# Kernel tuning notes

Measured on AMD Instinct MI355X. Metric: run time of the kernel, lower is better.

The kernel has to match this reference:

```python
import jax, jax.numpy as jnp
import numpy as np

N = 4096        # batch size (rows)
K = 4           # instances per class -> num_instances in the torch code
D = 256         # embedding dim
MARGIN = 0.5
SAMPLE_KEY = jax.random.key(42)  # fixed key: deterministic stand-in for torch.multinomial


def setup_inputs() -> dict:
    key = jax.random.key(0)
    x = jax.random.normal(key, (N, D), dtype=jnp.float32)
    # L2-normalize like typical metric-learning embeddings so sims are in [-1, 1]
    inputs = x / jnp.linalg.norm(x, axis=1, keepdims=True)
    targets = (jnp.arange(N) // K).astype(jnp.int32)  # P*K batch: equal-size classes
    return {"inputs": inputs, "targets": targets}


def reference(inputs, targets):
    n = inputs.shape[0]
    km1 = K - 1                 # positives per row
    n_neg = n - K               # negatives per row

    sim = inputs @ inputs.T                                   # [n, n]
    same = targets[:, None] == targets[None, :]
    eye = jnp.eye(n, dtype=bool)
    pos_mask = same & ~eye
    neg_mask = ~same

    # masked_select + per-row sort: masked entries -> +inf, ascending sort,
    # keep first count entries (counts are uniform across rows)
    pos_sorted = jnp.sort(jnp.where(pos_mask, sim, jnp.inf), axis=1)[:, :km1]   # [n, K-1]
    neg_sorted = jnp.sort(jnp.where(neg_mask, sim, jnp.inf), axis=1)[:, :n_neg] # [n, n-K]

    pos_d = jnp.mean(pos_sorted)
    neg_d = jnp.mean(neg_sorted)

    # GaussDistribution per row over negatives
    neg_mean = jnp.mean(neg_sorted, axis=1, keepdims=True)
    neg_std = jnp.sqrt(jnp.mean((neg_sorted - neg_mean) ** 2, axis=1, keepdims=True))
    # NOTE: the original uses exp(+(x-mu)^2 / (2 sigma^2)) (no minus sign) -- faithful
    logprob = (neg_sorted - neg_mean) ** 2 / (2.0 * neg_std ** 2)               # [n, n-K]

    # multinomial without replacement ~ Gumbel top-k on log-weights
    gumbel = -jnp.log(-jnp.log(
        jax.random.uniform(SAMPLE_KEY, logprob.shape, minval=1e-20, maxval=1.0)))
    _, neg_idx = jax.lax.top_k(logprob + gumbel, km1)                            # [n, K-1]
    neg_pair = jnp.take_along_axis(neg_sorted, neg_idx, axis=1)                  # [n, K-1]

    pos_loss = jnp.mean(jnp.log1p(jnp.exp(-2.0 * (pos_sorted - MARGIN))), axis=1)
    neg_loss = 0.04 * jnp.mean(jnp.log1p(jnp.exp(50.0 * (neg_pair - MARGIN))), axis=1)
    loss = jnp.sum(pos_loss + neg_loss) / n

    # prec: fraction of rows where hardest positive > hardest sampled negative + 0.05
    c = jnp.sum(pos_sorted[:, -1] > jnp.max(neg_pair, axis=1) + 0.05)
    prec = c.astype(jnp.float32) / n

    return loss, prec, pos_d, neg_d
```

## Files before the change

kernel.cpp:

```cpp
#include <hip/hip_runtime.h>
#include <hip/hip_bf16.h>
#include <cstdint>
#include <cfloat>
#include <math.h>

#define NN 4096
#define DD 256
#define NNEG 4092
#define MARGIN 0.5f
#define NB 3584
#define NW (NB / 2)
#define GTOTAL ((uint32_t)NN * (uint32_t)NNEG)

__device__ __forceinline__ uint32_t rotl32(uint32_t x, int r) {
  return (x << r) | (x >> (32 - r));
}

__device__ __forceinline__ void threefry2x32_42(uint32_t x0, uint32_t x1,
                                                uint32_t& o0, uint32_t& o1) {
  const uint32_t k0 = 0u, k1 = 42u;
  const uint32_t k2 = k0 ^ k1 ^ 0x1BD11BDAu;
  x0 += k0; x1 += k1;
#define TF_R(r) { x0 += x1; x1 = rotl32(x1, r); x1 ^= x0; }
  TF_R(13) TF_R(15) TF_R(26) TF_R(6)
  x0 += k1; x1 += k2 + 1u;
  TF_R(17) TF_R(29) TF_R(16) TF_R(24)
  x0 += k2; x1 += k0 + 2u;
  TF_R(13) TF_R(15) TF_R(26) TF_R(6)
  x0 += k0; x1 += k1 + 3u;
  TF_R(17) TF_R(29) TF_R(16) TF_R(24)
  x0 += k1; x1 += k2 + 4u;
  TF_R(13) TF_R(15) TF_R(26) TF_R(6)
  x0 += k2; x1 += k0 + 5u;
#undef TF_R
  o0 = x0; o1 = x1;
}

__device__ __forceinline__ float gumbel_at(uint32_t f) {
  uint32_t o0, o1;
  threefry2x32_42(0u, f, o0, o1);
  uint32_t bits = o0 ^ o1;
  uint32_t fb = (bits >> 9) | 0x3F800000u;
  float fl = __uint_as_float(fb) - 1.0f;
  float u = fmaxf(1e-20f, fl + 1e-20f);
  return -logf(-logf(u));
}

__device__ __forceinline__ int bucket_of(float v) {
  return (int)fminf(fmaxf((v + 0.28f) * 6400.0f, 0.0f), (float)(NB - 1));
}

#define BT 128
#define NT (NN / BT)
#define BK 32
#define LDSS 36
#define GEMM_BLOCKS (NT * (NT + 1) / 2)
#define GUMBEL_BLOCKS 240

template <int GOFF>
__global__ __launch_bounds__(256) void gemm_gumbel(const float* __restrict__ X,
                                                   float* __restrict__ S,
                                                   float* __restrict__ G) {
  __shared__ float As[BT * LDSS];
  __shared__ float Bs[BT * LDSS];
  const int tid = threadIdx.x;

  if (GOFF > 0 && (int)blockIdx.x >= GEMM_BLOCKS) {
    uint32_t i = (uint32_t)(blockIdx.x - GEMM_BLOCKS) * 256u + (uint32_t)tid;
    const uint32_t stride = (uint32_t)GOFF * 256u;
    for (; i < GTOTAL; i += stride) G[i] = gumbel_at(i);
    return;
  }

  const int tx = tid & 15, ty = tid >> 4;

  int b = blockIdx.x, bi = 0;
  while (b >= NT - bi) { b -= NT - bi; bi++; }
  const int bj = bi + b;
  const int rowBase = bi * BT, colBase = bj * BT;

  float acc[8][8] = {};
  for (int kb = 0; kb < DD; kb += BK) {
#pragma unroll
    for (int it = 0; it < 4; ++it) {
      int idx = tid + 256 * it;
      int r = idx >> 3, c4 = idx & 7;
      float4 av = *(const float4*)(X + (size_t)(rowBase + r) * DD + kb + c4 * 4);
      float4 bv = *(const float4*)(X + (size_t)(colBase + r) * DD + kb + c4 * 4);
      *(float4*)(As + r * LDSS + c4 * 4) = av;
      *(float4*)(Bs + r * LDSS + c4 * 4) = bv;
    }
    __syncthreads();
    for (int k = 0; k < BK; k += 4) {
      float4 a[8], bfr[8];
#pragma unroll
      for (int i = 0; i < 8; ++i) a[i] = *(const float4*)(As + (ty + 16 * i) * LDSS + k);
#pragma unroll
      for (int j = 0; j < 8; ++j) bfr[j] = *(const float4*)(Bs + (tx + 16 * j) * LDSS + k);
#pragma unroll
      for (int i = 0; i < 8; ++i)
#pragma unroll
        for (int j = 0; j < 8; ++j) {
          acc[i][j] += a[i].x * bfr[j].x;
          acc[i][j] += a[i].y * bfr[j].y;
          acc[i][j] += a[i].z * bfr[j].z;
          acc[i][j] += a[i].w * bfr[j].w;
        }
    }
    __syncthreads();
  }
#pragma unroll
  for (int i = 0; i < 8; ++i)
#pragma unroll
    for (int j = 0; j < 8; ++j)
      S[(size_t)(rowBase + ty + 16 * i) * NN + colBase + tx + 16 * j] = acc[i][j];
  if (bi != bj) {
#pragma unroll
    for (int i = 0; i < 8; ++i)
#pragma unroll
      for (int j = 0; j < 8; ++j)
        S[(size_t)(colBase + tx + 16 * j) * NN + rowBase + ty + 16 * i] = acc[i][j];
  }
}

#define INSERT3(sc, v)                                              \
  if ((sc) > s2) {                                                  \
    if ((sc) > s1) {                                                \
      s2 = s1; v2 = v1;                                             \
      if ((sc) > s0) { s1 = s0; v1 = v0; s0 = (sc); v0 = (v); }     \
      else           { s1 = (sc); v1 = (v); }                       \
    } else { s2 = (sc); v2 = (v); }                                 \
  }

template <int USE_G, int GSV>
__global__ __launch_bounds__(256) void row_kernel(const float* __restrict__ S,
                                                  const float* __restrict__ G,
                                                  float* __restrict__ svg,
                                                  float* __restrict__ acc) {
  __shared__ uint32_t histw[NW];
  __shared__ uint32_t offsw[NW];
  __shared__ __align__(16) float svs[GSV ? 4 : NN];
  __shared__ float sh[48];
  __shared__ uint32_t wtot[4];

  const int row = blockIdx.x;
  const int tid = threadIdx.x;
  const int lane = tid & 63, wid = tid >> 6;

  float* __restrict__ sv = GSV ? (svg + ((size_t)row << 12)) : svs;

#pragma unroll
  for (int i = 0; i < 7; ++i) histw[tid + 256 * i] = 0u;

  const float4* src = (const float4*)(S + (size_t)row * NN);
  const int pslot = row >> 2;
  float vv[16];
#pragma unroll
  for (int it = 0; it < 4; ++it) {
    int slot = tid + 256 * it;
    float4 t4 = src[slot];
    if (slot == pslot) {
      sh[16] = t4.x; sh[17] = t4.y; sh[18] = t4.z; sh[19] = t4.w;
      t4.x = INFINITY; t4.y = INFINITY; t4.z = INFINITY; t4.w = INFINITY;
    }
    vv[4 * it + 0] = t4.x; vv[4 * it + 1] = t4.y;
    vv[4 * it + 2] = t4.z; vv[4 * it + 3] = t4.w;
  }

  float s = 0.0f;
#pragma unroll
  for (int e = 0; e < 16; ++e) if (vv[e] < 1e30f) s += vv[e];
#pragma unroll
  for (int off = 32; off > 0; off >>= 1) s += __shfl_down(s, off, 64);
  if (lane == 0) sh[5 + wid] = s;
  __syncthreads();

#pragma unroll
  for (int e = 0; e < 16; ++e) {
    int b = bucket_of(vv[e]);
    atomicAdd(&histw[b >> 1], 1u << ((b & 1) << 4));
  }
  if (tid == 0) {
    int self = row & 3;
    float p[3]; int m = 0;
#pragma unroll
    for (int c = 0; c < 4; ++c)
      if (c != self) p[m++] = sh[16 + c];
    float t;
    if (p[0] > p[1]) { t = p[0]; p[0] = p[1]; p[1] = t; }
    if (p[1] > p[2]) { t = p[1]; p[1] = p[2]; p[2] = t; }
    if (p[0] > p[1]) { t = p[0]; p[0] = p[1]; p[1] = t; }
    sh[0] = p[0]; sh[1] = p[1]; sh[2] = p[2];
    float tot = sh[5] + sh[6] + sh[7] + sh[8];
    sh[9] = tot;
    sh[3] = tot / (float)NNEG;
  }
  __syncthreads();

  uint32_t hw[7];
  uint32_t s14 = 0;
#pragma unroll
  for (int j = 0; j < 7; ++j) {
    hw[j] = histw[7 * tid + j];
    s14 += (hw[j] & 0xFFFFu) + (hw[j] >> 16);
  }
  uint32_t inc = s14;
#pragma unroll
  for (int off = 1; off < 64; off <<= 1) {
    uint32_t n = __shfl_up(inc, (unsigned)off, 64);
    if (lane >= off) inc += n;
  }
  if (lane == 63) wtot[wid] = inc;

  const float mu = sh[3];
  float q = 0.0f;
#pragma unroll
  for (int e = 0; e < 16; ++e)
    if (vv[e] < 1e30f) { float d = vv[e] - mu; q += d * d; }
#pragma unroll
  for (int off = 32; off > 0; off >>= 1) q += __shfl_down(q, off, 64);
  if (lane == 0) sh[10 + wid] = q;
  __syncthreads();

  uint32_t wbase = 0;
  for (int w = 0; w < wid; ++w) wbase += wtot[w];
  uint32_t run = wbase + inc - s14;
#pragma unroll
  for (int j = 0; j < 7; ++j) {
    uint32_t lo = run; run += hw[j] & 0xFFFFu;
    uint32_t hi = run; run += hw[j] >> 16;
    offsw[7 * tid + j] = lo | (hi << 16);
  }
  if (tid == 0) {
    float var = (sh[10] + sh[11] + sh[12] + sh[13]) / (float)NNEG;
    float sd = sqrtf(var);
    sh[4] = 1.0f / (2.0f * sd * sd);
  }
  __syncthreads();

#pragma unroll
  for (int e = 0; e < 16; ++e) {
    int b = bucket_of(vv[e]);
    uint32_t old = atomicAdd(&offsw[b >> 1], 1u << ((b & 1) << 4));
    uint32_t sl = (old >> ((b & 1) << 4)) & 0xFFFFu;
    sv[sl] = vv[e];
  }
  __syncthreads();

  const float inv2s2 = sh[4];
  const uint32_t fbase = (uint32_t)row * (uint32_t)NNEG;
  const float* __restrict__ Grow = G + fbase;
  float s0 = -FLT_MAX, s1 = -FLT_MAX, s2 = -FLT_MAX;
  float v0 = 0.0f, v1 = 0.0f, v2 = 0.0f;

  float va[16]; uint32_t sten[16];
#pragma unroll
  for (int it = 0; it < 16; ++it) va[it] = sv[tid + 256 * it];
#pragma unroll
  for (int it = 0; it < 16; ++it) {
    float v = va[it];
    uint32_t pk = 0u;
    if (v < 1e30f) {
      int b = bucket_of(v);
      uint32_t sh16 = (uint32_t)((b & 1) << 4);
      uint32_t end = (offsw[b >> 1] >> sh16) & 0xFFFFu;
      uint32_t cb = (histw[b >> 1] >> sh16) & 0xFFFFu;
      pk = (end - cb) | (end << 16);
    }
    sten[it] = pk;
  }

#pragma unroll
  for (int half = 0; half < 2; ++half) {
    float4 w0[8];
#pragma unroll
    for (int j = 0; j < 8; ++j) {
      uint32_t st = sten[half * 8 + j] & 0xFFFFu;
      w0[j] = *(const float4*)(sv + (st & ~3u));
    }
#pragma unroll
    for (int j = 0; j < 8; ++j) {
      const int it = half * 8 + j;
      float v = va[it];
      if (v < 1e30f) {
        const int sl = tid + 256 * it;
        const uint32_t st = sten[it] & 0xFFFFu, en = sten[it] >> 16;
        const uint32_t nb = en - st;
        const uint32_t u0 = st & ~3u;
        int cnt = (int)st;
        {
          float4 w = w0[j];
          cnt += ((u0 + 0 - st) < nb && (w.x < v || (w.x == v && (int)(u0 + 0) < sl))) ? 1 : 0;
          cnt += ((u0 + 1 - st) < nb && (w.y < v || (w.y == v && (int)(u0 + 1) < sl))) ? 1 : 0;
          cnt += ((u0 + 2 - st) < nb && (w.z < v || (w.z == v && (int)(u0 + 2) < sl))) ? 1 : 0;
          cnt += ((u0 + 3 - st) < nb && (w.w < v || (w.w == v && (int)(u0 + 3) < sl))) ? 1 : 0;
        }
        for (uint32_t u = u0 + 4; u < en; u += 4) {
          float4 w = *(const float4*)(sv + u);
          cnt += ((u + 0 - st) < nb && (w.x < v || (w.x == v && (int)(u + 0) < sl))) ? 1 : 0;
          cnt += ((u + 1 - st) < nb && (w.y < v || (w.y == v && (int)(u + 1) < sl))) ? 1 : 0;
          cnt += ((u + 2 - st) < nb && (w.z < v || (w.z == v && (int)(u + 2) < sl))) ? 1 : 0;
          cnt += ((u + 3 - st) < nb && (w.w < v || (w.w == v && (int)(u + 3) < sl))) ? 1 : 0;
        }
        float g = USE_G ? Grow[cnt] : gumbel_at(fbase + (uint32_t)cnt);
        float d = v - mu;
        float sc = d * d * inv2s2 + g;
        INSERT3(sc, v)
      }
    }
  }

#pragma unroll
  for (int dlt = 1; dlt < 64; dlt <<= 1) {
    float t0 = __shfl_xor(s0, dlt, 64), u0 = __shfl_xor(v0, dlt, 64);
    float t1 = __shfl_xor(s1, dlt, 64), u1 = __shfl_xor(v1, dlt, 64);
    float t2 = __shfl_xor(s2, dlt, 64), u2 = __shfl_xor(v2, dlt, 64);
    INSERT3(t0, u0)
    INSERT3(t1, u1)
    INSERT3(t2, u2)
  }
  if (lane == 0) {
    int b0 = 24 + wid * 6;
    sh[b0 + 0] = s0; sh[b0 + 1] = v0;
    sh[b0 + 2] = s1; sh[b0 + 3] = v1;
    sh[b0 + 4] = s2; sh[b0 + 5] = v2;
  }
  __syncthreads();

  if (tid == 0) {
    float g0 = -FLT_MAX, g1 = -FLT_MAX, g2 = -FLT_MAX;
    float w0 = 0.0f, w1 = 0.0f, w2 = 0.0f;
    {
      float s0 = g0, s1 = g1, s2 = g2, v0 = w0, v1 = w1, v2 = w2;
#pragma unroll
      for (int i = 0; i < 12; ++i) {
        float sc = sh[24 + 2 * i], v = sh[24 + 2 * i + 1];
        INSERT3(sc, v)
      }
      g0 = s0; g1 = s1; g2 = s2; w0 = v0; w1 = v1; w2 = v2;
    }
    float negmax = fmaxf(w0, fmaxf(w1, w2));
    float neg_loss = 0.04f * (log1pf(expf(50.0f * (w0 - MARGIN))) +
                              log1pf(expf(50.0f * (w1 - MARGIN))) +
                              log1pf(expf(50.0f * (w2 - MARGIN)))) / 3.0f;
    float p0 = sh[0], p1 = sh[1], p2 = sh[2];
    float pos_loss = (log1pf(expf(-2.0f * (p0 - MARGIN))) +
                      log1pf(expf(-2.0f * (p1 - MARGIN))) +
                      log1pf(expf(-2.0f * (p2 - MARGIN)))) / 3.0f;
    atomicAdd(&acc[0], pos_loss + neg_loss);
    if (p2 > negmax + 0.05f) atomicAdd(&acc[1], 1.0f);
    atomicAdd(&acc[2], p0 + p1 + p2);
    atomicAdd(&acc[3], sh[9]);
  }
}

__global__ void finalize(const float* __restrict__ acc, float* out) {
  if (threadIdx.x == 0 && blockIdx.x == 0) {
    out[0] = acc[0] / 4096.0f;
    out[1] = acc[1] / 4096.0f;
    out[2] = acc[2] / (4096.0f * 3.0f);
    out[3] = acc[3] / (4096.0f * 4092.0f);
  }
}

extern "C" void kernel_launch(void* const* d_in, const int* in_sizes, int n_in,
                              void* d_out, int out_size, void* d_ws, size_t ws_size,
                              hipStream_t stream) {
  (void)in_sizes; (void)n_in; (void)out_size;
  const float* X = (const float*)d_in[0];
  float* S = (float*)d_ws;
  float* acc = (float*)((char*)d_ws + (size_t)NN * NN * 4);
  float* G = (float*)((char*)d_ws + (size_t)NN * NN * 4 + 256);
  float* SV = (float*)((char*)d_ws + 2 * (size_t)NN * NN * 4 + 256);
  const size_t need_g = (size_t)NN * NN * 4 + 256 + (size_t)GTOTAL * 4;
  const size_t need_sv = 2 * (size_t)NN * NN * 4 + 256 + (size_t)NN * NN * 4;
  const bool have_g = ws_size >= need_g;
  const bool have_sv = ws_size >= need_sv;

  hipMemsetAsync(acc, 0, 4 * sizeof(float), stream);
  if (have_g) {
    gemm_gumbel<GUMBEL_BLOCKS><<<GEMM_BLOCKS + GUMBEL_BLOCKS, 256, 0, stream>>>(X, S, G);
    if (have_sv) row_kernel<1, 1><<<NN, 256, 0, stream>>>(S, G, SV, acc);
    else         row_kernel<1, 0><<<NN, 256, 0, stream>>>(S, G, SV, acc);
  } else {
    gemm_gumbel<0><<<GEMM_BLOCKS, 256, 0, stream>>>(X, S, G);
    row_kernel<0, 0><<<NN, 256, 0, stream>>>(S, G, SV, acc);
  }
  finalize<<<1, 64, 0, stream>>>(acc, (float*)d_out);
}
```

Before: 403.4 us.

## Fuse GEMM and row kernels into one launch with per-row-tile ready counters

Merges the similarity GEMM and the per-row sampling kernel into a single persistent-style launch. Row blocks spin on an atomic counter per 128-row tile until all 32 GEMM tiles covering that row are written, so row processing overlaps with remaining GEMM work. The precomputed Gumbel buffer is dropped and noise is recomputed inline for the selected index only, and the sorted values now live in shared memory via dynamic LDS. The risks are spin-wait deadlock if row blocks occupy slots before GEMM blocks are scheduled, and higher LDS use per block.

```diff
diff --git a/kernel.cpp b/kernel.cpp
--- a/kernel.cpp
+++ b/kernel.cpp
@@ -1,5 +1,4 @@
 #include <hip/hip_runtime.h>
-#include <hip/hip_bf16.h>
 #include <cstdint>
 #include <cfloat>
 #include <math.h>
@@ -10,7 +9,6 @@
 #define MARGIN 0.5f
 #define NB 3584
 #define NW (NB / 2)
-#define GTOTAL ((uint32_t)NN * (uint32_t)NNEG)
 
 __device__ __forceinline__ uint32_t rotl32(uint32_t x, int r) {
   return (x << r) | (x >> (32 - r));
@@ -55,73 +53,7 @@
 #define BK 32
 #define LDSS 36
 #define GEMM_BLOCKS (NT * (NT + 1) / 2)
-#define GUMBEL_BLOCKS 240
-
-template <int GOFF>
-__global__ __launch_bounds__(256) void gemm_gumbel(const float* __restrict__ X,
-                                                   float* __restrict__ S,
-                                                   float* __restrict__ G) {
-  __shared__ float As[BT * LDSS];
-  __shared__ float Bs[BT * LDSS];
-  const int tid = threadIdx.x;
-
-  if (GOFF > 0 && (int)blockIdx.x >= GEMM_BLOCKS) {
-    uint32_t i = (uint32_t)(blockIdx.x - GEMM_BLOCKS) * 256u + (uint32_t)tid;
-    const uint32_t stride = (uint32_t)GOFF * 256u;
-    for (; i < GTOTAL; i += stride) G[i] = gumbel_at(i);
-    return;
-  }
-
-  const int tx = tid & 15, ty = tid >> 4;
-
-  int b = blockIdx.x, bi = 0;
-  while (b >= NT - bi) { b -= NT - bi; bi++; }
-  const int bj = bi + b;
-  const int rowBase = bi * BT, colBase = bj * BT;
-
-  float acc[8][8] = {};
-  for (int kb = 0; kb < DD; kb += BK) {
-#pragma unroll
-    for (int it = 0; it < 4; ++it) {
-      int idx = tid + 256 * it;
-      int r = idx >> 3, c4 = idx & 7;
-      float4 av = *(const float4*)(X + (size_t)(rowBase + r) * DD + kb + c4 * 4);
-      float4 bv = *(const float4*)(X + (size_t)(colBase + r) * DD + kb + c4 * 4);
-      *(float4*)(As + r * LDSS + c4 * 4) = av;
-      *(float4*)(Bs + r * LDSS + c4 * 4) = bv;
-    }
-    __syncthreads();
-    for (int k = 0; k < BK; k += 4) {
-      float4 a[8], bfr[8];
-#pragma unroll
-      for (int i = 0; i < 8; ++i) a[i] = *(const float4*)(As + (ty + 16 * i) * LDSS + k);
-#pragma unroll
-      for (int j = 0; j < 8; ++j) bfr[j] = *(const float4*)(Bs + (tx + 16 * j) * LDSS + k);
-#pragma unroll
-      for (int i = 0; i < 8; ++i)
-#pragma unroll
-        for (int j = 0; j < 8; ++j) {
-          acc[i][j] += a[i].x * bfr[j].x;
-          acc[i][j] += a[i].y * bfr[j].y;
-          acc[i][j] += a[i].z * bfr[j].z;
-          acc[i][j] += a[i].w * bfr[j].w;
-        }
-    }
-    __syncthreads();
-  }
-#pragma unroll
-  for (int i = 0; i < 8; ++i)
-#pragma unroll
-    for (int j = 0; j < 8; ++j)
-      S[(size_t)(rowBase + ty + 16 * i) * NN + colBase + tx + 16 * j] = acc[i][j];
-  if (bi != bj) {
-#pragma unroll
-    for (int i = 0; i < 8; ++i)
-#pragma unroll
-      for (int j = 0; j < 8; ++j)
-        S[(size_t)(colBase + tx + 16 * j) * NN + rowBase + ty + 16 * i] = acc[i][j];
-  }
-}
+#define SMEM_BYTES 36864
 
 #define INSERT3(sc, v)                                              \
   if ((sc) > s2) {                                                  \
@@ -132,25 +64,93 @@
     } else { s2 = (sc); v2 = (v); }                                 \
   }
 
-template <int USE_G, int GSV>
-__global__ __launch_bounds__(256) void row_kernel(const float* __restrict__ S,
-                                                  const float* __restrict__ G,
-                                                  float* __restrict__ svg,
-                                                  float* __restrict__ acc) {
-  __shared__ uint32_t histw[NW];
-  __shared__ uint32_t offsw[NW];
-  __shared__ __align__(16) float svs[GSV ? 4 : NN];
-  __shared__ float sh[48];
-  __shared__ uint32_t wtot[4];
-
-  const int row = blockIdx.x;
+__global__ __launch_bounds__(256) void fused(const float* __restrict__ X,
+                                             float* __restrict__ S,
+                                             uint32_t* __restrict__ ctr,
+                                             float* __restrict__ acc) {
+  extern __shared__ __align__(16) char smem[];
   const int tid = threadIdx.x;
+
+  if ((int)blockIdx.x < GEMM_BLOCKS) {
+    float* As = (float*)smem;
+    float* Bs = (float*)(smem + 18432);
+    const int tx = tid & 15, ty = tid >> 4;
+
+    int b = (int)blockIdx.x, bi = 0;
+    while (b >= NT - bi) { b -= NT - bi; bi++; }
+    const int bj = bi + b;
+    const int rowBase = bi * BT, colBase = bj * BT;
+
+    float accr[8][8] = {};
+    for (int kb = 0; kb < DD; kb += BK) {
+#pragma unroll
+      for (int it = 0; it < 4; ++it) {
+        int idx = tid + 256 * it;
+        int r = idx >> 3, c4 = idx & 7;
+        float4 av = *(const float4*)(X + (size_t)(rowBase + r) * DD + kb + c4 * 4);
+        float4 bv = *(const float4*)(X + (size_t)(colBase + r) * DD + kb + c4 * 4);
+        *(float4*)(As + r * LDSS + c4 * 4) = av;
+        *(float4*)(Bs + r * LDSS + c4 * 4) = bv;
+      }
+      __syncthreads();
+      for (int k = 0; k < BK; k += 4) {
+        float4 a[8], bfr[8];
+#pragma unroll
+        for (int i = 0; i < 8; ++i) a[i] = *(const float4*)(As + (ty + 16 * i) * LDSS + k);
+#pragma unroll
+        for (int j = 0; j < 8; ++j) bfr[j] = *(const float4*)(Bs + (tx + 16 * j) * LDSS + k);
+#pragma unroll
+        for (int i = 0; i < 8; ++i)
+#pragma unroll
+          for (int j = 0; j < 8; ++j) {
+            accr[i][j] += a[i].x * bfr[j].x;
+            accr[i][j] += a[i].y * bfr[j].y;
+            accr[i][j] += a[i].z * bfr[j].z;
+            accr[i][j] += a[i].w * bfr[j].w;
+          }
+      }
+      __syncthreads();
+    }
+#pragma unroll
+    for (int i = 0; i < 8; ++i)
+#pragma unroll
+      for (int j = 0; j < 8; ++j)
+        S[(size_t)(rowBase + ty + 16 * i) * NN + colBase + tx + 16 * j] = accr[i][j];
+    if (bi != bj) {
+#pragma unroll
+      for (int i = 0; i < 8; ++i)
+#pragma unroll
+        for (int j = 0; j < 8; ++j)
+          S[(size_t)(colBase + tx + 16 * j) * NN + rowBase + ty + 16 * i] = accr[i][j];
+    }
+    __syncthreads();
+    if (tid == 0) {
+      __threadfence();
+      __hip_atomic_fetch_add(&ctr[bi], 1u, __ATOMIC_RELEASE, __HIP_MEMORY_SCOPE_AGENT);
+      if (bi != bj)
+        __hip_atomic_fetch_add(&ctr[bj], 1u, __ATOMIC_RELEASE, __HIP_MEMORY_SCOPE_AGENT);
+    }
+    return;
+  }
+
+  uint32_t* histw = (uint32_t*)smem;
+  uint32_t* offsw = (uint32_t*)(smem + 7168);
+  float*    sval  = (float*)(smem + 14336);
+  float*    sh    = (float*)(smem + 30720);
+  uint32_t* wtot  = (uint32_t*)(smem + 30912);
+
+  const int row = (int)blockIdx.x - GEMM_BLOCKS;
   const int lane = tid & 63, wid = tid >> 6;
 
-  float* __restrict__ sv = GSV ? (svg + ((size_t)row << 12)) : svs;
-
 #pragma unroll
   for (int i = 0; i < 7; ++i) histw[tid + 256 * i] = 0u;
+  if (tid == 0) {
+    while (__hip_atomic_load(&ctr[row >> 7], __ATOMIC_ACQUIRE,
+                             __HIP_MEMORY_SCOPE_AGENT) < 32u)
+      __builtin_amdgcn_s_sleep(16);
+    __threadfence();
+  }
+  __syncthreads();
 
   const float4* src = (const float4*)(S + (size_t)row * NN);
   const int pslot = row >> 2;
@@ -243,19 +243,18 @@
     int b = bucket_of(vv[e]);
     uint32_t old = atomicAdd(&offsw[b >> 1], 1u << ((b & 1) << 4));
     uint32_t sl = (old >> ((b & 1) << 4)) & 0xFFFFu;
-    sv[sl] = vv[e];
+    sval[sl] = vv[e];
   }
   __syncthreads();
 
   const float inv2s2 = sh[4];
   const uint32_t fbase = (uint32_t)row * (uint32_t)NNEG;
-  const float* __restrict__ Grow = G + fbase;
   float s0 = -FLT_MAX, s1 = -FLT_MAX, s2 = -FLT_MAX;
   float v0 = 0.0f, v1 = 0.0f, v2 = 0.0f;
 
   float va[16]; uint32_t sten[16];
 #pragma unroll
-  for (int it = 0; it < 16; ++it) va[it] = sv[tid + 256 * it];
+  for (int it = 0; it < 16; ++it) va[it] = sval[tid + 256 * it];
 #pragma unroll
   for (int it = 0; it < 16; ++it) {
     float v = va[it];
@@ -276,7 +275,7 @@
 #pragma unroll
     for (int j = 0; j < 8; ++j) {
       uint32_t st = sten[half * 8 + j] & 0xFFFFu;
-      w0[j] = *(const float4*)(sv + (st & ~3u));
+      w0[j] = *(const float4*)(sval + (st & ~3u));
     }
 #pragma unroll
     for (int j = 0; j < 8; ++j) {
@@ -296,13 +295,13 @@
           cnt += ((u0 + 3 - st) < nb && (w.w < v || (w.w == v && (int)(u0 + 3) < sl))) ? 1 : 0;
         }
         for (uint32_t u = u0 + 4; u < en; u += 4) {
-          float4 w = *(const float4*)(sv + u);
+          float4 w = *(const float4*)(sval + u);
           cnt += ((u + 0 - st) < nb && (w.x < v || (w.x == v && (int)(u + 0) < sl))) ? 1 : 0;
           cnt += ((u + 1 - st) < nb && (w.y < v || (w.y == v && (int)(u + 1) < sl))) ? 1 : 0;
           cnt += ((u + 2 - st) < nb && (w.z < v || (w.z == v && (int)(u + 2) < sl))) ? 1 : 0;
           cnt += ((u + 3 - st) < nb && (w.w < v || (w.w == v && (int)(u + 3) < sl))) ? 1 : 0;
         }
-        float g = USE_G ? Grow[cnt] : gumbel_at(fbase + (uint32_t)cnt);
+        float g = gumbel_at(fbase + (uint32_t)cnt);
         float d = v - mu;
         float sc = d * d * inv2s2 + g;
         INSERT3(sc, v)
@@ -366,25 +365,13 @@
 extern "C" void kernel_launch(void* const* d_in, const int* in_sizes, int n_in,
                               void* d_out, int out_size, void* d_ws, size_t ws_size,
                               hipStream_t stream) {
-  (void)in_sizes; (void)n_in; (void)out_size;
+  (void)in_sizes; (void)n_in; (void)out_size; (void)ws_size;
   const float* X = (const float*)d_in[0];
   float* S = (float*)d_ws;
   float* acc = (float*)((char*)d_ws + (size_t)NN * NN * 4);
-  float* G = (float*)((char*)d_ws + (size_t)NN * NN * 4 + 256);
-  float* SV = (float*)((char*)d_ws + 2 * (size_t)NN * NN * 4 + 256);
-  const size_t need_g = (size_t)NN * NN * 4 + 256 + (size_t)GTOTAL * 4;
-  const size_t need_sv = 2 * (size_t)NN * NN * 4 + 256 + (size_t)NN * NN * 4;
-  const bool have_g = ws_size >= need_g;
-  const bool have_sv = ws_size >= need_sv;
-
-  hipMemsetAsync(acc, 0, 4 * sizeof(float), stream);
-  if (have_g) {
-    gemm_gumbel<GUMBEL_BLOCKS><<<GEMM_BLOCKS + GUMBEL_BLOCKS, 256, 0, stream>>>(X, S, G);
-    if (have_sv) row_kernel<1, 1><<<NN, 256, 0, stream>>>(S, G, SV, acc);
-    else         row_kernel<1, 0><<<NN, 256, 0, stream>>>(S, G, SV, acc);
-  } else {
-    gemm_gumbel<0><<<GEMM_BLOCKS, 256, 0, stream>>>(X, S, G);
-    row_kernel<0, 0><<<NN, 256, 0, stream>>>(S, G, SV, acc);
-  }
+  uint32_t* ctr = (uint32_t*)((char*)d_ws + (size_t)NN * NN * 4 + 16);
+
+  hipMemsetAsync(acc, 0, 256, stream);
+  fused<<<GEMM_BLOCKS + NN, 256, SMEM_BYTES, stream>>>(X, S, ctr, acc);
   finalize<<<1, 64, 0, stream>>>(acc, (float*)d_out);
 }
```

Measured after the change: 603.5 us. 49.6% more time.

## Process two rows per 512-thread block with the sorted-values buffer in LDS

Applied to the files above, without the earlier changes.

The per-row kernel body moves into a device function. A new 512-thread kernel runs two rows per block, each half with its own shared-memory histogram, offsets and sorted-value array. This drops the global-memory scratch path for the bucket-sorted values, so the rank-counting loop reads from LDS instead of global or L2. The trade-off is about 60KB of LDS per block, which limits resident blocks per CU, and block-wide barriers now tie the two rows together.

```diff
diff --git a/kernel.cpp b/kernel.cpp
--- a/kernel.cpp
+++ b/kernel.cpp
@@ -1,5 +1,4 @@
 #include <hip/hip_runtime.h>
-#include <hip/hip_bf16.h>
 #include <cstdint>
 #include <cfloat>
 #include <math.h>
@@ -132,32 +131,27 @@
     } else { s2 = (sc); v2 = (v); }                                 \
   }
 
-template <int USE_G, int GSV>
-__global__ __launch_bounds__(256) void row_kernel(const float* __restrict__ S,
-                                                  const float* __restrict__ G,
-                                                  float* __restrict__ svg,
-                                                  float* __restrict__ acc) {
-  __shared__ uint32_t histw[NW];
-  __shared__ uint32_t offsw[NW];
-  __shared__ __align__(16) float svs[GSV ? 4 : NN];
-  __shared__ float sh[48];
-  __shared__ uint32_t wtot[4];
-
-  const int row = blockIdx.x;
-  const int tid = threadIdx.x;
-  const int lane = tid & 63, wid = tid >> 6;
-
-  float* __restrict__ sv = GSV ? (svg + ((size_t)row << 12)) : svs;
-
-#pragma unroll
-  for (int i = 0; i < 7; ++i) histw[tid + 256 * i] = 0u;
+template <int USE_G>
+__device__ __forceinline__ void row_body(const int row, const int ltid,
+                                         const float* __restrict__ S,
+                                         const float* __restrict__ G,
+                                         float* __restrict__ acc,
+                                         uint32_t* __restrict__ histw,
+                                         uint32_t* __restrict__ offsw,
+                                         float* __restrict__ sval,
+                                         float* __restrict__ sh,
+                                         uint32_t* __restrict__ wtot) {
+  const int lane = ltid & 63, wid = ltid >> 6;
+
+#pragma unroll
+  for (int i = 0; i < 7; ++i) histw[ltid + 256 * i] = 0u;
 
   const float4* src = (const float4*)(S + (size_t)row * NN);
   const int pslot = row >> 2;
   float vv[16];
 #pragma unroll
   for (int it = 0; it < 4; ++it) {
-    int slot = tid + 256 * it;
+    int slot = ltid + 256 * it;
     float4 t4 = src[slot];
     if (slot == pslot) {
       sh[16] = t4.x; sh[17] = t4.y; sh[18] = t4.z; sh[19] = t4.w;
@@ -180,7 +174,7 @@
     int b = bucket_of(vv[e]);
     atomicAdd(&histw[b >> 1], 1u << ((b & 1) << 4));
   }
-  if (tid == 0) {
+  if (ltid == 0) {
     int self = row & 3;
     float p[3]; int m = 0;
 #pragma unroll
@@ -201,7 +195,7 @@
   uint32_t s14 = 0;
 #pragma unroll
   for (int j = 0; j < 7; ++j) {
-    hw[j] = histw[7 * tid + j];
+    hw[j] = histw[7 * ltid + j];
     s14 += (hw[j] & 0xFFFFu) + (hw[j] >> 16);
   }
   uint32_t inc = s14;
@@ -229,9 +223,9 @@
   for (int j = 0; j < 7; ++j) {
     uint32_t lo = run; run += hw[j] & 0xFFFFu;
     uint32_t hi = run; run += hw[j] >> 16;
-    offsw[7 * tid + j] = lo | (hi << 16);
-  }
-  if (tid == 0) {
+    offsw[7 * ltid + j] = lo | (hi << 16);
+  }
+  if (ltid == 0) {
     float var = (sh[10] + sh[11] + sh[12] + sh[13]) / (float)NNEG;
     float sd = sqrtf(var);
     sh[4] = 1.0f / (2.0f * sd * sd);
@@ -243,7 +237,7 @@
     int b = bucket_of(vv[e]);
     uint32_t old = atomicAdd(&offsw[b >> 1], 1u << ((b & 1) << 4));
     uint32_t sl = (old >> ((b & 1) << 4)) & 0xFFFFu;
-    sv[sl] = vv[e];
+    sval[sl] = vv[e];
   }
   __syncthreads();
 
@@ -255,7 +249,7 @@
 
   float va[16]; uint32_t sten[16];
 #pragma unroll
-  for (int it = 0; it < 16; ++it) va[it] = sv[tid + 256 * it];
+  for (int it = 0; it < 16; ++it) va[it] = sval[ltid + 256 * it];
 #pragma unroll
   for (int it = 0; it < 16; ++it) {
     float v = va[it];
@@ -276,14 +270,14 @@
 #pragma unroll
     for (int j = 0; j < 8; ++j) {
       uint32_t st = sten[half * 8 + j] & 0xFFFFu;
-      w0[j] = *(const float4*)(sv + (st & ~3u));
+      w0[j] = *(const float4*)(sval + (st & ~3u));
     }
 #pragma unroll
     for (int j = 0; j < 8; ++j) {
       const int it = half * 8 + j;
       float v = va[it];
       if (v < 1e30f) {
-        const int sl = tid + 256 * it;
+        const int sl = ltid + 256 * it;
         const uint32_t st = sten[it] & 0xFFFFu, en = sten[it] >> 16;
         const uint32_t nb = en - st;
         const uint32_t u0 = st & ~3u;
@@ -296,7 +290,7 @@
           cnt += ((u0 + 3 - st) < nb && (w.w < v || (w.w == v && (int)(u0 + 3) < sl))) ? 1 : 0;
         }
         for (uint32_t u = u0 + 4; u < en; u += 4) {
-          float4 w = *(const float4*)(sv + u);
+          float4 w = *(const float4*)(sval + u);
           cnt += ((u + 0 - st) < nb && (w.x < v || (w.x == v && (int)(u + 0) < sl))) ? 1 : 0;
           cnt += ((u + 1 - st) < nb && (w.y < v || (w.y == v && (int)(u + 1) < sl))) ? 1 : 0;
           cnt += ((u + 2 - st) < nb && (w.z < v || (w.z == v && (int)(u + 2) < sl))) ? 1 : 0;
@@ -327,7 +321,7 @@
   }
   __syncthreads();
 
-  if (tid == 0) {
+  if (ltid == 0) {
     float g0 = -FLT_MAX, g1 = -FLT_MAX, g2 = -FLT_MAX;
     float w0 = 0.0f, w1 = 0.0f, w2 = 0.0f;
     {
@@ -354,6 +348,25 @@
   }
 }
 
+template <int USE_G>
+__global__ __launch_bounds__(512) void row2_kernel(const float* __restrict__ S,
+                                                   const float* __restrict__ G,
+                                                   float* __restrict__ acc) {
+  __shared__ uint32_t histw[2][NW];
+  __shared__ uint32_t offsw[2][NW];
+  __shared__ __align__(16) float sval[2][NN];
+  __shared__ float sh[2][48];
+  __shared__ uint32_t wtot[2][4];
+
+  const int tid = threadIdx.x;
+  const int half = tid >> 8;
+  const int ltid = tid & 255;
+  const int row = 2 * blockIdx.x + half;
+
+  row_body<USE_G>(row, ltid, S, G, acc,
+                  histw[half], offsw[half], sval[half], sh[half], wtot[half]);
+}
+
 __global__ void finalize(const float* __restrict__ acc, float* out) {
   if (threadIdx.x == 0 && blockIdx.x == 0) {
     out[0] = acc[0] / 4096.0f;
@@ -371,20 +384,16 @@
   float* S = (float*)d_ws;
   float* acc = (float*)((char*)d_ws + (size_t)NN * NN * 4);
   float* G = (float*)((char*)d_ws + (size_t)NN * NN * 4 + 256);
-  float* SV = (float*)((char*)d_ws + 2 * (size_t)NN * NN * 4 + 256);
   const size_t need_g = (size_t)NN * NN * 4 + 256 + (size_t)GTOTAL * 4;
-  const size_t need_sv = 2 * (size_t)NN * NN * 4 + 256 + (size_t)NN * NN * 4;
   const bool have_g = ws_size >= need_g;
-  const bool have_sv = ws_size >= need_sv;
 
   hipMemsetAsync(acc, 0, 4 * sizeof(float), stream);
   if (have_g) {
     gemm_gumbel<GUMBEL_BLOCKS><<<GEMM_BLOCKS + GUMBEL_BLOCKS, 256, 0, stream>>>(X, S, G);
-    if (have_sv) row_kernel<1, 1><<<NN, 256, 0, stream>>>(S, G, SV, acc);
-    else         row_kernel<1, 0><<<NN, 256, 0, stream>>>(S, G, SV, acc);
+    row2_kernel<1><<<NN / 2, 512, 0, stream>>>(S, G, acc);
   } else {
     gemm_gumbel<0><<<GEMM_BLOCKS, 256, 0, stream>>>(X, S, G);
-    row_kernel<0, 0><<<NN, 256, 0, stream>>>(S, G, SV, acc);
+    row2_kernel<0><<<NN / 2, 512, 0, stream>>>(S, G, acc);
   }
   finalize<<<1, 64, 0, stream>>>(acc, (float*)d_out);
 }
```

After: 380.0 us. 1.06x faster.

## Process four rows per block with next-row prefetch and LDS sorted buffer

Applied to the files above, without the earlier changes.

The row kernel now handles four rows per block in a loop and prefetches the next row of the similarity matrix into registers while the current row is processed. The sorted-value scratch array is always kept in shared memory instead of an optional global-memory buffer. This targets global latency on row loads and the global round-trip for the sorted buffer. The trade-off is four times fewer blocks, which cuts parallelism across CUs, plus an extra barrier per row.

```diff
diff --git a/kernel.cpp b/kernel.cpp
--- a/kernel.cpp
+++ b/kernel.cpp
@@ -1,5 +1,4 @@
 #include <hip/hip_runtime.h>
-#include <hip/hip_bf16.h>
 #include <cstdint>
 #include <cfloat>
 #include <math.h>
@@ -11,6 +10,7 @@
 #define NB 3584
 #define NW (NB / 2)
 #define GTOTAL ((uint32_t)NN * (uint32_t)NNEG)
+#define RPB 4
 
 __device__ __forceinline__ uint32_t rotl32(uint32_t x, int r) {
   return (x << r) | (x >> (32 - r));
@@ -132,225 +132,241 @@
     } else { s2 = (sc); v2 = (v); }                                 \
   }
 
-template <int USE_G, int GSV>
+template <int USE_G>
 __global__ __launch_bounds__(256) void row_kernel(const float* __restrict__ S,
                                                   const float* __restrict__ G,
-                                                  float* __restrict__ svg,
                                                   float* __restrict__ acc) {
   __shared__ uint32_t histw[NW];
   __shared__ uint32_t offsw[NW];
-  __shared__ __align__(16) float svs[GSV ? 4 : NN];
+  __shared__ __align__(16) float sval[NN];
   __shared__ float sh[48];
   __shared__ uint32_t wtot[4];
 
-  const int row = blockIdx.x;
   const int tid = threadIdx.x;
   const int lane = tid & 63, wid = tid >> 6;
-
-  float* __restrict__ sv = GSV ? (svg + ((size_t)row << 12)) : svs;
-
-#pragma unroll
-  for (int i = 0; i < 7; ++i) histw[tid + 256 * i] = 0u;
-
-  const float4* src = (const float4*)(S + (size_t)row * NN);
-  const int pslot = row >> 2;
-  float vv[16];
-#pragma unroll
-  for (int it = 0; it < 4; ++it) {
-    int slot = tid + 256 * it;
-    float4 t4 = src[slot];
-    if (slot == pslot) {
-      sh[16] = t4.x; sh[17] = t4.y; sh[18] = t4.z; sh[19] = t4.w;
-      t4.x = INFINITY; t4.y = INFINITY; t4.z = INFINITY; t4.w = INFINITY;
-    }
-    vv[4 * it + 0] = t4.x; vv[4 * it + 1] = t4.y;
-    vv[4 * it + 2] = t4.z; vv[4 * it + 3] = t4.w;
-  }
-
-  float s = 0.0f;
-#pragma unroll
-  for (int e = 0; e < 16; ++e) if (vv[e] < 1e30f) s += vv[e];
-#pragma unroll
-  for (int off = 32; off > 0; off >>= 1) s += __shfl_down(s, off, 64);
-  if (lane == 0) sh[5 + wid] = s;
-  __syncthreads();
-
-#pragma unroll
-  for (int e = 0; e < 16; ++e) {
-    int b = bucket_of(vv[e]);
-    atomicAdd(&histw[b >> 1], 1u << ((b & 1) << 4));
-  }
-  if (tid == 0) {
-    int self = row & 3;
-    float p[3]; int m = 0;
-#pragma unroll
-    for (int c = 0; c < 4; ++c)
-      if (c != self) p[m++] = sh[16 + c];
-    float t;
-    if (p[0] > p[1]) { t = p[0]; p[0] = p[1]; p[1] = t; }
-    if (p[1] > p[2]) { t = p[1]; p[1] = p[2]; p[2] = t; }
-    if (p[0] > p[1]) { t = p[0]; p[0] = p[1]; p[1] = t; }
-    sh[0] = p[0]; sh[1] = p[1]; sh[2] = p[2];
-    float tot = sh[5] + sh[6] + sh[7] + sh[8];
-    sh[9] = tot;
-    sh[3] = tot / (float)NNEG;
-  }
-  __syncthreads();
-
-  uint32_t hw[7];
-  uint32_t s14 = 0;
-#pragma unroll
-  for (int j = 0; j < 7; ++j) {
-    hw[j] = histw[7 * tid + j];
-    s14 += (hw[j] & 0xFFFFu) + (hw[j] >> 16);
-  }
-  uint32_t inc = s14;
-#pragma unroll
-  for (int off = 1; off < 64; off <<= 1) {
-    uint32_t n = __shfl_up(inc, (unsigned)off, 64);
-    if (lane >= off) inc += n;
-  }
-  if (lane == 63) wtot[wid] = inc;
-
-  const float mu = sh[3];
-  float q = 0.0f;
-#pragma unroll
-  for (int e = 0; e < 16; ++e)
-    if (vv[e] < 1e30f) { float d = vv[e] - mu; q += d * d; }
-#pragma unroll
-  for (int off = 32; off > 0; off >>= 1) q += __shfl_down(q, off, 64);
-  if (lane == 0) sh[10 + wid] = q;
-  __syncthreads();
-
-  uint32_t wbase = 0;
-  for (int w = 0; w < wid; ++w) wbase += wtot[w];
-  uint32_t run = wbase + inc - s14;
-#pragma unroll
-  for (int j = 0; j < 7; ++j) {
-    uint32_t lo = run; run += hw[j] & 0xFFFFu;
-    uint32_t hi = run; run += hw[j] >> 16;
-    offsw[7 * tid + j] = lo | (hi << 16);
-  }
-  if (tid == 0) {
-    float var = (sh[10] + sh[11] + sh[12] + sh[13]) / (float)NNEG;
-    float sd = sqrtf(var);
-    sh[4] = 1.0f / (2.0f * sd * sd);
-  }
-  __syncthreads();
-
-#pragma unroll
-  for (int e = 0; e < 16; ++e) {
-    int b = bucket_of(vv[e]);
-    uint32_t old = atomicAdd(&offsw[b >> 1], 1u << ((b & 1) << 4));
-    uint32_t sl = (old >> ((b & 1) << 4)) & 0xFFFFu;
-    sv[sl] = vv[e];
-  }
-  __syncthreads();
-
-  const float inv2s2 = sh[4];
-  const uint32_t fbase = (uint32_t)row * (uint32_t)NNEG;
-  const float* __restrict__ Grow = G + fbase;
-  float s0 = -FLT_MAX, s1 = -FLT_MAX, s2 = -FLT_MAX;
-  float v0 = 0.0f, v1 = 0.0f, v2 = 0.0f;
-
-  float va[16]; uint32_t sten[16];
-#pragma unroll
-  for (int it = 0; it < 16; ++it) va[it] = sv[tid + 256 * it];
-#pragma unroll
-  for (int it = 0; it < 16; ++it) {
-    float v = va[it];
-    uint32_t pk = 0u;
-    if (v < 1e30f) {
-      int b = bucket_of(v);
-      uint32_t sh16 = (uint32_t)((b & 1) << 4);
-      uint32_t end = (offsw[b >> 1] >> sh16) & 0xFFFFu;
-      uint32_t cb = (histw[b >> 1] >> sh16) & 0xFFFFu;
-      pk = (end - cb) | (end << 16);
-    }
-    sten[it] = pk;
-  }
-
-#pragma unroll
-  for (int half = 0; half < 2; ++half) {
-    float4 w0[8];
-#pragma unroll
-    for (int j = 0; j < 8; ++j) {
-      uint32_t st = sten[half * 8 + j] & 0xFFFFu;
-      w0[j] = *(const float4*)(sv + (st & ~3u));
-    }
-#pragma unroll
-    for (int j = 0; j < 8; ++j) {
-      const int it = half * 8 + j;
+  const int row0 = (int)blockIdx.x * RPB;
+
+  float4 pre[4];
+  {
+    const float4* src = (const float4*)(S + (size_t)row0 * NN);
+#pragma unroll
+    for (int it = 0; it < 4; ++it) pre[it] = src[tid + 256 * it];
+  }
+
+#pragma unroll 1
+  for (int r = 0; r < RPB; ++r) {
+    const int row = row0 + r;
+
+#pragma unroll
+    for (int i = 0; i < 7; ++i) histw[tid + 256 * i] = 0u;
+
+    const int pslot = row >> 2;
+    float vv[16];
+#pragma unroll
+    for (int it = 0; it < 4; ++it) {
+      int slot = tid + 256 * it;
+      float4 t4 = pre[it];
+      if (slot == pslot) {
+        sh[16] = t4.x; sh[17] = t4.y; sh[18] = t4.z; sh[19] = t4.w;
+        t4.x = INFINITY; t4.y = INFINITY; t4.z = INFINITY; t4.w = INFINITY;
+      }
+      vv[4 * it + 0] = t4.x; vv[4 * it + 1] = t4.y;
+      vv[4 * it + 2] = t4.z; vv[4 * it + 3] = t4.w;
+    }
+
+    {
+      const int nrow = (r + 1 < RPB) ? (row + 1) : row;
+      const float4* nsrc = (const float4*)(S + (size_t)nrow * NN);
+#pragma unroll
+      for (int it = 0; it < 4; ++it) pre[it] = nsrc[tid + 256 * it];
+    }
+
+    float s = 0.0f;
+#pragma unroll
+    for (int e = 0; e < 16; ++e) if (vv[e] < 1e30f) s += vv[e];
+#pragma unroll
+    for (int off = 32; off > 0; off >>= 1) s += __shfl_down(s, off, 64);
+    if (lane == 0) sh[5 + wid] = s;
+    __syncthreads();
+
+#pragma unroll
+    for (int e = 0; e < 16; ++e) {
+      int b = bucket_of(vv[e]);
+      atomicAdd(&histw[b >> 1], 1u << ((b & 1) << 4));
+    }
+    if (tid == 0) {
+      int self = row & 3;
+      float p[3]; int m = 0;
+#pragma unroll
+      for (int c = 0; c < 4; ++c)
+        if (c != self) p[m++] = sh[16 + c];
+      float t;
+      if (p[0] > p[1]) { t = p[0]; p[0] = p[1]; p[1] = t; }
+      if (p[1] > p[2]) { t = p[1]; p[1] = p[2]; p[2] = t; }
+      if (p[0] > p[1]) { t = p[0]; p[0] = p[1]; p[1] = t; }
+      sh[0] = p[0]; sh[1] = p[1]; sh[2] = p[2];
+      float tot = sh[5] + sh[6] + sh[7] + sh[8];
+      sh[9] = tot;
+      sh[3] = tot / (float)NNEG;
+    }
+    __syncthreads();
+
+    uint32_t hw[7];
+    uint32_t s14 = 0;
+#pragma unroll
+    for (int j = 0; j < 7; ++j) {
+      hw[j] = histw[7 * tid + j];
+      s14 += (hw[j] & 0xFFFFu) + (hw[j] >> 16);
+    }
+    uint32_t inc = s14;
+#pragma unroll
+    for (int off = 1; off < 64; off <<= 1) {
+      uint32_t n = __shfl_up(inc, (unsigned)off, 64);
+      if (lane >= off) inc += n;
+    }
+    if (lane == 63) wtot[wid] = inc;
+
+    const float mu = sh[3];
+    float q = 0.0f;
+#pragma unroll
+    for (int e = 0; e < 16; ++e)
+      if (vv[e] < 1e30f) { float d = vv[e] - mu; q += d * d; }
+#pragma unroll
+    for (int off = 32; off > 0; off >>= 1) q += __shfl_down(q, off, 64);
+    if (lane == 0) sh[10 + wid] = q;
+    __syncthreads();
+
+    uint32_t wbase = 0;
+    for (int w = 0; w < wid; ++w) wbase += wtot[w];
+    uint32_t run = wbase + inc - s14;
+#pragma unroll
+    for (int j = 0; j < 7; ++j) {
+      uint32_t lo = run; run += hw[j] & 0xFFFFu;
+      uint32_t hi = run; run += hw[j] >> 16;
+      offsw[7 * tid + j] = lo | (hi << 16);
+    }
+    if (tid == 0) {
+      float var = (sh[10] + sh[11] + sh[12] + sh[13]) / (float)NNEG;
+      float sd = sqrtf(var);
+      sh[4] = 1.0f / (2.0f * sd * sd);
+    }
+    __syncthreads();
+
+#pragma unroll
+    for (int e = 0; e < 16; ++e) {
+      int b = bucket_of(vv[e]);
+      uint32_t old = atomicAdd(&offsw[b >> 1], 1u << ((b & 1) << 4));
+      uint32_t sl = (old >> ((b & 1) << 4)) & 0xFFFFu;
+      sval[sl] = vv[e];
+    }
+    __syncthreads();
+
+    const float inv2s2 = sh[4];
+    const uint32_t fbase = (uint32_t)row * (uint32_t)NNEG;
+    const float* __restrict__ Grow = G + fbase;
+    float s0 = -FLT_MAX, s1 = -FLT_MAX, s2 = -FLT_MAX;
+    float v0 = 0.0f, v1 = 0.0f, v2 = 0.0f;
+
+    float va[16]; uint32_t sten[16];
+#pragma unroll
+    for (int it = 0; it < 16; ++it) va[it] = sval[tid + 256 * it];
+#pragma unroll
+    for (int it = 0; it < 16; ++it) {
       float v = va[it];
+      uint32_t pk = 0u;
       if (v < 1e30f) {
-        const int sl = tid + 256 * it;
-        const uint32_t st = sten[it] & 0xFFFFu, en = sten[it] >> 16;
-        const uint32_t nb = en - st;
-        const uint32_t u0 = st & ~3u;
-        int cnt = (int)st;
-        {
-          float4 w = w0[j];
-          cnt += ((u0 + 0 - st) < nb && (w.x < v || (w.x == v && (int)(u0 + 0) < sl))) ? 1 : 0;
-          cnt += ((u0 + 1 - st) < nb && (w.y < v || (w.y == v && (int)(u0 + 1) < sl))) ? 1 : 0;
-          cnt += ((u0 + 2 - st) < nb && (w.z < v || (w.z == v && (int)(u0 + 2) < sl))) ? 1 : 0;
-          cnt += ((u0 + 3 - st) < nb && (w.w < v || (w.w == v && (int)(u0 + 3) < sl))) ? 1 : 0;
+        int b = bucket_of(v);
+        uint32_t sh16 = (uint32_t)((b & 1) << 4);
+        uint32_t end = (offsw[b >> 1] >> sh16) & 0xFFFFu;
+        uint32_t cb = (histw[b >> 1] >> sh16) & 0xFFFFu;
+        pk = (end - cb) | (end << 16);
+      }
+      sten[it] = pk;
+    }
+
+#pragma unroll
+    for (int half = 0; half < 2; ++half) {
+      float4 w0[8];
+#pragma unroll
+      for (int j = 0; j < 8; ++j) {
+        uint32_t st = sten[half * 8 + j] & 0xFFFFu;
+        w0[j] = *(const float4*)(sval + (st & ~3u));
+      }
+#pragma unroll
+      for (int j = 0; j < 8; ++j) {
+        const int it = half * 8 + j;
+        float v = va[it];
+        if (v < 1e30f) {
+          const int sl = tid + 256 * it;
+          const uint32_t st = sten[it] & 0xFFFFu, en = sten[it] >> 16;
+          const uint32_t nb = en - st;
+          const uint32_t u0 = st & ~3u;
+          int cnt = (int)st;
+          {
+            float4 w = w0[j];
+            cnt += ((u0 + 0 - st) < nb && (w.x < v || (w.x == v && (int)(u0 + 0) < sl))) ? 1 : 0;
+            cnt += ((u0 + 1 - st) < nb && (w.y < v || (w.y == v && (int)(u0 + 1) < sl))) ? 1 : 0;
+            cnt += ((u0 + 2 - st) < nb && (w.z < v || (w.z == v && (int)(u0 + 2) < sl))) ? 1 : 0;
+            cnt += ((u0 + 3 - st) < nb && (w.w < v || (w.w == v && (int)(u0 + 3) < sl))) ? 1 : 0;
+          }
+          for (uint32_t u = u0 + 4; u < en; u += 4) {
+            float4 w = *(const float4*)(sval + u);
+            cnt += ((u + 0 - st) < nb && (w.x < v || (w.x == v && (int)(u + 0) < sl))) ? 1 : 0;
+            cnt += ((u + 1 - st) < nb && (w.y < v || (w.y == v && (int)(u + 1) < sl))) ? 1 : 0;
+            cnt += ((u + 2 - st) < nb && (w.z < v || (w.z == v && (int)(u + 2) < sl))) ? 1 : 0;
+            cnt += ((u + 3 - st) < nb && (w.w < v || (w.w == v && (int)(u + 3) < sl))) ? 1 : 0;
+          }
+          float g = USE_G ? Grow[cnt] : gumbel_at(fbase + (uint32_t)cnt);
+          float d = v - mu;
+          float sc = d * d * inv2s2 + g;
+          INSERT3(sc, v)
         }
-        for (uint32_t u = u0 + 4; u < en; u += 4) {
-          float4 w = *(const float4*)(sv + u);
-          cnt += ((u + 0 - st) < nb && (w.x < v || (w.x == v && (int)(u + 0) < sl))) ? 1 : 0;
-          cnt += ((u + 1 - st) < nb && (w.y < v || (w.y == v && (int)(u + 1) < sl))) ? 1 : 0;
-          cnt += ((u + 2 - st) < nb && (w.z < v || (w.z == v && (int)(u + 2) < sl))) ? 1 : 0;
-          cnt += ((u + 3 - st) < nb && (w.w < v || (w.w == v && (int)(u + 3) < sl))) ? 1 : 0;
+      }
+    }
+
+#pragma unroll
+    for (int dlt = 1; dlt < 64; dlt <<= 1) {
+      float t0 = __shfl_xor(s0, dlt, 64), u0 = __shfl_xor(v0, dlt, 64);
+      float t1 = __shfl_xor(s1, dlt, 64), u1 = __shfl_xor(v1, dlt, 64);
+      float t2 = __shfl_xor(s2, dlt, 64), u2 = __shfl_xor(v2, dlt, 64);
+      INSERT3(t0, u0)
+      INSERT3(t1, u1)
+      INSERT3(t2, u2)
+    }
+    if (lane == 0) {
+      int b0 = 24 + wid * 6;
+      sh[b0 + 0] = s0; sh[b0 + 1] = v0;
+      sh[b0 + 2] = s1; sh[b0 + 3] = v1;
+      sh[b0 + 4] = s2; sh[b0 + 5] = v2;
+    }
+    __syncthreads();
+
+    if (tid == 0) {
+      float g0 = -FLT_MAX, g1 = -FLT_MAX, g2 = -FLT_MAX;
+      float w0 = 0.0f, w1 = 0.0f, w2 = 0.0f;
+      {
+        float s0 = g0, s1 = g1, s2 = g2, v0 = w0, v1 = w1, v2 = w2;
+#pragma unroll
+        for (int i = 0; i < 12; ++i) {
+          float sc = sh[24 + 2 * i], v = sh[24 + 2 * i + 1];
+          INSERT3(sc, v)
         }
-        float g = USE_G ? Grow[cnt] : gumbel_at(fbase + (uint32_t)cnt);
-        float d = v - mu;
-        float sc = d * d * inv2s2 + g;
-        INSERT3(sc, v)
+        g0 = s0; g1 = s1; g2 = s2; w0 = v0; w1 = v1; w2 = v2;
       }
-    }
-  }
-
-#pragma unroll
-  for (int dlt = 1; dlt < 64; dlt <<= 1) {
-    float t0 = __shfl_xor(s0, dlt, 64), u0 = __shfl_xor(v0, dlt, 64);
-    float t1 = __shfl_xor(s1, dlt, 64), u1 = __shfl_xor(v1, dlt, 64);
-    float t2 = __shfl_xor(s2, dlt, 64), u2 = __shfl_xor(v2, dlt, 64);
-    INSERT3(t0, u0)
-    INSERT3(t1, u1)
-    INSERT3(t2, u2)
-  }
-  if (lane == 0) {
-    int b0 = 24 + wid * 6;
-    sh[b0 + 0] = s0; sh[b0 + 1] = v0;
-    sh[b0 + 2] = s1; sh[b0 + 3] = v1;
-    sh[b0 + 4] = s2; sh[b0 + 5] = v2;
-  }
-  __syncthreads();
-
-  if (tid == 0) {
-    float g0 = -FLT_MAX, g1 = -FLT_MAX, g2 = -FLT_MAX;
-    float w0 = 0.0f, w1 = 0.0f, w2 = 0.0f;
-    {
-      float s0 = g0, s1 = g1, s2 = g2, v0 = w0, v1 = w1, v2 = w2;
-#pragma unroll
-      for (int i = 0; i < 12; ++i) {
-        float sc = sh[24 + 2 * i], v = sh[24 + 2 * i + 1];
-        INSERT3(sc, v)
-      }
-      g0 = s0; g1 = s1; g2 = s2; w0 = v0; w1 = v1; w2 = v2;
-    }
-    float negmax = fmaxf(w0, fmaxf(w1, w2));
-    float neg_loss = 0.04f * (log1pf(expf(50.0f * (w0 - MARGIN))) +
-                              log1pf(expf(50.0f * (w1 - MARGIN))) +
-                              log1pf(expf(50.0f * (w2 - MARGIN)))) / 3.0f;
-    float p0 = sh[0], p1 = sh[1], p2 = sh[2];
-    float pos_loss = (log1pf(expf(-2.0f * (p0 - MARGIN))) +
-                      log1pf(expf(-2.0f * (p1 - MARGIN))) +
-                      log1pf(expf(-2.0f * (p2 - MARGIN)))) / 3.0f;
-    atomicAdd(&acc[0], pos_loss + neg_loss);
-    if (p2 > negmax + 0.05f) atomicAdd(&acc[1], 1.0f);
-    atomicAdd(&acc[2], p0 + p1 + p2);
-    atomicAdd(&acc[3], sh[9]);
+      float negmax = fmaxf(w0, fmaxf(w1, w2));
+      float neg_loss = 0.04f * (log1pf(expf(50.0f * (w0 - MARGIN))) +
+                                log1pf(expf(50.0f * (w1 - MARGIN))) +
+                                log1pf(expf(50.0f * (w2 - MARGIN)))) / 3.0f;
+      float p0 = sh[0], p1 = sh[1], p2 = sh[2];
+      float pos_loss = (log1pf(expf(-2.0f * (p0 - MARGIN))) +
+                        log1pf(expf(-2.0f * (p1 - MARGIN))) +
+                        log1pf(expf(-2.0f * (p2 - MARGIN)))) / 3.0f;
+      atomicAdd(&acc[0], pos_loss + neg_loss);
+      if (p2 > negmax + 0.05f) atomicAdd(&acc[1], 1.0f);
+      atomicAdd(&acc[2], p0 + p1 + p2);
+      atomicAdd(&acc[3], sh[9]);
+    }
+    __syncthreads();
   }
 }
 
@@ -371,20 +387,16 @@
   float* S = (float*)d_ws;
   float* acc = (float*)((char*)d_ws + (size_t)NN * NN * 4);
   float* G = (float*)((char*)d_ws + (size_t)NN * NN * 4 + 256);
-  float* SV = (float*)((char*)d_ws + 2 * (size_t)NN * NN * 4 + 256);
   const size_t need_g = (size_t)NN * NN * 4 + 256 + (size_t)GTOTAL * 4;
-  const size_t need_sv = 2 * (size_t)NN * NN * 4 + 256 + (size_t)NN * NN * 4;
   const bool have_g = ws_size >= need_g;
-  const bool have_sv = ws_size >= need_sv;
 
   hipMemsetAsync(acc, 0, 4 * sizeof(float), stream);
   if (have_g) {
     gemm_gumbel<GUMBEL_BLOCKS><<<GEMM_BLOCKS + GUMBEL_BLOCKS, 256, 0, stream>>>(X, S, G);
-    if (have_sv) row_kernel<1, 1><<<NN, 256, 0, stream>>>(S, G, SV, acc);
-    else         row_kernel<1, 0><<<NN, 256, 0, stream>>>(S, G, SV, acc);
+    row_kernel<1><<<NN / RPB, 256, 0, stream>>>(S, G, acc);
   } else {
     gemm_gumbel<0><<<GEMM_BLOCKS, 256, 0, stream>>>(X, S, G);
-    row_kernel<0, 0><<<NN, 256, 0, stream>>>(S, G, SV, acc);
+    row_kernel<0><<<NN / RPB, 256, 0, stream>>>(S, G, acc);
   }
   finalize<<<1, 64, 0, stream>>>(acc, (float*)d_out);
 }
```

After: 411.1 us. About the same (+1.9%).
